# Kernel optimization log

Measured on AMD Instinct MI355X. Metric: run time of the kernel, lower is better.

## Reference

```python
import jax, jax.numpy as jnp
import numpy as np

B, S, DIN, DIM, H = 2, 2304, 1024, 1024, 16
HEAD_DIM = DIM // H            # 64
ROT_DIM = HEAD_DIM             # partial_rotary_factor = 1
BASE = 10000.0
EPS = 1e-6


def setup_inputs() -> dict:
    key = jax.random.key(0)
    ks = jax.random.split(key, 6)
    return {
        "input": jax.random.normal(ks[0], (B, S, DIN), dtype=jnp.float32),
        "qkv_w": jax.random.normal(ks[1], (3 * DIM, DIN), dtype=jnp.float32) * 0.02,
        "qkv_b": jnp.zeros((3 * DIM,), dtype=jnp.float32),
        "q_scale": jnp.ones((DIM,), dtype=jnp.float32),
        "k_scale": jnp.ones((DIM,), dtype=jnp.float32),
        "proj_w": jax.random.normal(ks[2], (DIN, DIM), dtype=jnp.float32) * 0.02,
        "proj_b": jnp.zeros((DIN,), dtype=jnp.float32),
        "height": 48,
        "width": 48,
    }


def _rms_norm(x, scale):
    # RMSNorm over the full inner dim (QKNorm), learned scale
    var = jnp.mean(x * x, axis=-1, keepdims=True)
    return x * jax.lax.rsqrt(var + EPS) * scale


def _rope_1d(x, pos):
    # x: (b, n, h, d_ax), pos: (n,) float; rotate_half-style RoPE
    d = x.shape[-1]
    inv_freq = 1.0 / (BASE ** (jnp.arange(0, d, 2, dtype=jnp.float32) / d))  # (d/2,)
    ang = pos[:, None] * inv_freq                                            # (n, d/2)
    cos = jnp.concatenate([jnp.cos(ang), jnp.cos(ang)], axis=-1)[None, :, None, :]
    sin = jnp.concatenate([jnp.sin(ang), jnp.sin(ang)], axis=-1)[None, :, None, :]
    x1, x2 = jnp.split(x, 2, axis=-1)
    rot = jnp.concatenate([-x2, x1], axis=-1)
    return x * cos + rot * sin


def _rope_2d(x, height, width):
    # axial 2D RoPE: first half of rotary dims keyed by row, second half by col
    n = height * width
    idx = jnp.arange(n, dtype=jnp.float32)
    rows = jnp.floor(idx / width)
    cols = jnp.mod(idx, width)
    half = ROT_DIM // 2
    x_r = _rope_1d(x[..., :half], rows)
    x_c = _rope_1d(x[..., half:ROT_DIM], cols)
    return jnp.concatenate([x_r, x_c, x[..., ROT_DIM:]], axis=-1)


def reference(input, qkv_w, qkv_b, q_scale, k_scale, proj_w, proj_b, height, width):
    b, n, _ = input.shape
    qkv = input @ qkv_w.T + qkv_b                       # (b, n, 3*dim)
    q, k, v = jnp.split(qkv, 3, axis=-1)
    q = _rms_norm(q, q_scale)
    k = _rms_norm(k, k_scale)
    # (b, n, h, d)
    q = q.reshape(b, n, H, HEAD_DIM)
    k = k.reshape(b, n, H, HEAD_DIM)
    v = v.reshape(b, n, H, HEAD_DIM)
    q = _rope_2d(q, height, width)
    k = _rope_2d(k, height, width)
    scale = HEAD_DIM ** (-0.5)
    # (b, h, q, k)
    scores = jnp.einsum("bqhd,bkhd->bhqk", q, k) * scale
    attn = jax.nn.softmax(scores, axis=-1)
    out = jnp.einsum("bhqk,bkhd->bqhd", attn, v)        # (b, n, h, d)
    out = out.reshape(b, n, DIM)
    return out @ proj_w.T + proj_b
```

## Files before the change

kernel.cpp:

```cpp
#include <hip/hip_runtime.h>
#include <math.h>

#define BB   2
#define SS   2304
#define DINC 1024
#define DIMC 1024
#define HH   16
#define HD   64

typedef _Float16 half_t;
typedef __attribute__((ext_vector_type(4))) _Float16 half4;
typedef __attribute__((ext_vector_type(8))) _Float16 half8;
typedef __attribute__((ext_vector_type(4))) float    f32x4;

#define LOG2E 1.44269504088896340736f
#define EXP2(x) __builtin_amdgcn_exp2f(x)

#define GLOAD_LDS16(gp, lp)                                                     \
    __builtin_amdgcn_global_load_lds(                                           \
        (const __attribute__((address_space(1))) void*)(gp),                    \
        (__attribute__((address_space(3))) void*)(lp), 16, 0, 0)

template<int RB>
__device__ __forceinline__
void conv_body(const float* __restrict__ src, half_t* __restrict__ dst,
               int K, int mb, int kb, int t)
{
    constexpr int NG = RB * 32 / 1024;
    const float* sp0 = src + (size_t)mb * RB * K + kb * 32;
    half_t*      dp0 = dst + ((size_t)mb * (K >> 5) + kb) * (RB * 32);
    #pragma unroll
    for (int g = 0; g < NG; ++g) {
        const int e  = g * 1024 + t * 4;
        const int mm = e >> 5, kk = e & 31;
        float4 v = *(const float4*)(sp0 + (size_t)mm * K + kk);
        dp0[e + 0] = (half_t)v.x; dp0[e + 1] = (half_t)v.y;
        dp0[e + 2] = (half_t)v.z; dp0[e + 3] = (half_t)v.w;
    }
}

__global__ __launch_bounds__(256)
void convert_all_f16(const float* __restrict__ input, const float* __restrict__ qkv_w,
                     const float* __restrict__ proj_w, half_t* __restrict__ Ah,
                     half_t* __restrict__ Bh1, half_t* __restrict__ Bh2)
{
    const int bx = blockIdx.x;
    const int kb = blockIdx.y;
    const int t  = threadIdx.x;
    if (bx < 24)      conv_body<192>(input, Ah,  DINC, bx,      kb, t);
    else if (bx < 56) conv_body<96>(qkv_w, Bh1, DINC, bx - 24, kb, t);
    else              conv_body<64>(proj_w, Bh2, DIMC, bx - 56, kb, t);
}

__global__ __launch_bounds__(256, 3)
void gemm_mfma192(const half_t* __restrict__ Ah, const half_t* __restrict__ Bh,
                  const float* __restrict__ bias, half_t* __restrict__ Cout)
{
    const int t    = threadIdx.x;
    const int w    = t >> 6;
    const int lane = t & 63;
    const int l15  = lane & 15, quad = lane >> 4;
    const int wr   = w >> 1;
    const int wc   = w & 1;
    const int mb   = blockIdx.y;
    const int nb   = blockIdx.x;

    __shared__ __align__(16) half_t As[2][6144];
    __shared__ __align__(16) half_t Bs[2][3072];

    f32x4 acc[6][3];
    #pragma unroll
    for (int mt = 0; mt < 6; ++mt)
        #pragma unroll
        for (int nt = 0; nt < 3; ++nt) acc[mt][nt] = (f32x4){0.f, 0.f, 0.f, 0.f};

    const half_t* atile = Ah + (size_t)mb * 32 * 6144;
    const half_t* btile = Bh + (size_t)nb * 32 * 3072;

    for (int kb = 0; kb < 32; kb += 2) {
        #pragma unroll
        for (int u = 0; u < 2; ++u) {
            const half_t* at = atile + (size_t)(kb + u) * 6144;
            const half_t* bt = btile + (size_t)(kb + u) * 3072;
            for (int ch = w; ch < 18; ch += 4) {
                if (ch < 12) GLOAD_LDS16(at + ch * 512 + lane * 8, &As[u][ch * 512]);
                else         GLOAD_LDS16(bt + (ch - 12) * 512 + lane * 8,
                                         &Bs[u][(ch - 12) * 512]);
            }
        }
        __syncthreads();

        #pragma unroll
        for (int u = 0; u < 2; ++u) {
            half8 af[6], bf[3];
            #pragma unroll
            for (int mt = 0; mt < 6; ++mt)
                af[mt] = *(const half8*)(&As[u][(wr * 96 + mt * 16 + l15) * 32 + quad * 8]);
            #pragma unroll
            for (int nt = 0; nt < 3; ++nt)
                bf[nt] = *(const half8*)(&Bs[u][(wc * 48 + nt * 16 + l15) * 32 + quad * 8]);
            #pragma unroll
            for (int mt = 0; mt < 6; ++mt)
                #pragma unroll
                for (int nt = 0; nt < 3; ++nt)
                    acc[mt][nt] = __builtin_amdgcn_mfma_f32_16x16x32_f16(
                        af[mt], bf[nt], acc[mt][nt], 0, 0, 0);
        }
        __syncthreads();
    }

    const int bm = mb * 192, bn = nb * 96;
    #pragma unroll
    for (int nt = 0; nt < 3; ++nt) {
        const int n  = bn + wc * 48 + nt * 16 + l15;
        const float bv = bias[n];
        #pragma unroll
        for (int mt = 0; mt < 6; ++mt) {
            const int m0 = bm + wr * 96 + mt * 16 + quad * 4;
            #pragma unroll
            for (int rg = 0; rg < 4; ++rg)
                Cout[(size_t)(m0 + rg) * 3072 + n] = (half_t)(acc[mt][nt][rg] + bv);
        }
    }
}

template<int BN, bool OUT_HALF>
__global__ __launch_bounds__(256)
void gemm_mfma(const half_t* __restrict__ Ah, const half_t* __restrict__ Bh,
               const float* __restrict__ bias, void* __restrict__ Cout,
               int M, int N, int K)
{
    constexpr int MT = (BN == 128) ? 4 : 2;
    constexpr int NT = 4;
    const int KB = K >> 5;
    __shared__ half_t As[8192];
    __shared__ half_t Bs[2 * BN * 32];

    const int t    = threadIdx.x;
    const int w    = t >> 6;
    const int lane = t & 63;
    const int l15  = lane & 15, quad = lane >> 4;
    const int wr   = (BN == 128) ? (w >> 1) : w;
    const int wc   = (BN == 128) ? (w & 1) : 0;
    const int mb   = blockIdx.y, nb = blockIdx.x;

    f32x4 acc[MT][NT];
    #pragma unroll
    for (int mt = 0; mt < MT; ++mt)
        #pragma unroll
        for (int nt = 0; nt < NT; ++nt) acc[mt][nt] = (f32x4){0.f, 0.f, 0.f, 0.f};

    const half_t* atile = Ah + (size_t)mb * KB * 4096;
    const half_t* btile = Bh + (size_t)nb * KB * (BN * 32);

    for (int kb = 0; kb < KB; kb += 2) {
        #pragma unroll
        for (int u = 0; u < 2; ++u) {
            const half_t* at = atile + (size_t)(kb + u) * 4096;
            const half_t* bt = btile + (size_t)(kb + u) * (BN * 32);
            #pragma unroll
            for (int v = 0; v < 2; ++v) {
                const int ch = w * 2 + v;
                GLOAD_LDS16(at + ch * 512 + lane * 8, As + u * 4096 + ch * 512);
            }
            GLOAD_LDS16(bt + w * 512 + lane * 8, Bs + u * (BN * 32) + w * 512);
        }
        __syncthreads();

        #pragma unroll
        for (int u = 0; u < 2; ++u) {
            half8 af[MT], bf[NT];
            #pragma unroll
            for (int mt = 0; mt < MT; ++mt)
                af[mt] = *(const half8*)(As + u * 4096
                                         + (wr * (MT * 16) + mt * 16 + l15) * 32 + quad * 8);
            #pragma unroll
            for (int nt = 0; nt < NT; ++nt)
                bf[nt] = *(const half8*)(Bs + u * (BN * 32)
                                         + (wc * 64 + nt * 16 + l15) * 32 + quad * 8);
            #pragma unroll
            for (int mt = 0; mt < MT; ++mt)
                #pragma unroll
                for (int nt = 0; nt < NT; ++nt)
                    acc[mt][nt] = __builtin_amdgcn_mfma_f32_16x16x32_f16(
                        af[mt], bf[nt], acc[mt][nt], 0, 0, 0);
        }
        __syncthreads();
    }

    const int bm = mb * 128, bn = nb * BN;
    #pragma unroll
    for (int nt = 0; nt < NT; ++nt) {
        const int n  = bn + wc * 64 + nt * 16 + l15;
        const float bv = bias[n];
        #pragma unroll
        for (int mt = 0; mt < MT; ++mt) {
            const int m0 = bm + wr * (MT * 16) + mt * 16 + quad * 4;
            #pragma unroll
            for (int rg = 0; rg < 4; ++rg) {
                const float v = acc[mt][nt][rg] + bv;
                if (OUT_HALF) ((half_t*)Cout)[(size_t)(m0 + rg) * N + n] = (half_t)v;
                else          ((float*) Cout)[(size_t)(m0 + rg) * N + n] = v;
            }
        }
    }
}

__global__ __launch_bounds__(256)
void normrope_v8(half_t* __restrict__ qkvh, const float* __restrict__ q_scale,
                 const float* __restrict__ k_scale, const int* __restrict__ wptr,
                 half_t* __restrict__ Kf, half_t* __restrict__ Vf)
{
    const int token = blockIdx.x;
    const int s     = token % SS;
    const int b     = token / SS;
    const int w     = *wptr;
    const int t     = threadIdx.x;
    const float rowp = (float)(s / w);
    const float colp = (float)(s % w);

    half_t* base = qkvh + (size_t)token * 3072;

    const int c    = s >> 5;
    const int slot = s & 31;
    const int ktile = (slot >> 2) & 1;
    const int krow  = ((slot >> 3) << 2) + (slot & 3);

    {
        half4 v4 = *(const half4*)(base + 2048 + 4 * t);
        const int dabs0 = 4 * t;
        const int h  = dabs0 >> 6;
        const int sl3 = slot >> 3, sl7 = slot & 7;
        half_t* vdst = Vf + ((size_t)(b * HH + h) * 72 + c) * 2048;
        #pragma unroll
        for (int ii = 0; ii < 4; ++ii) {
            const int d = (dabs0 + ii) & 63;
            vdst[(d >> 4) * 512 + (sl3 * 16 + (d & 15)) * 8 + sl7] = v4[ii];
        }
    }

    __shared__ float buf[DIMC];
    __shared__ float red[4];
    __shared__ __align__(16) half_t obuf[DIMC];

    #pragma unroll
    for (int sel = 0; sel < 2; ++sel) {
        half_t* row = base + sel * DIMC;
        const float* scp = sel ? k_scale : q_scale;

        half4 xh = *(const half4*)(row + 4 * t);
        float x0 = (float)xh[0], x1 = (float)xh[1], x2 = (float)xh[2], x3 = (float)xh[3];
        float ss = x0 * x0 + x1 * x1 + x2 * x2 + x3 * x3;
        #pragma unroll
        for (int o = 32; o >= 1; o >>= 1) ss += __shfl_xor(ss, o);
        if ((t & 63) == 0) red[t >> 6] = ss;
        __syncthreads();

        const float rinv = rsqrtf((red[0] + red[1] + red[2] + red[3]) * (1.0f / DIMC) + 1e-6f);
        float4 g = *(const float4*)(scp + 4 * t);
        buf[4 * t + 0] = x0 * rinv * g.x;
        buf[4 * t + 1] = x1 * rinv * g.y;
        buf[4 * t + 2] = x2 * rinv * g.z;
        buf[4 * t + 3] = x3 * rinv * g.w;
        __syncthreads();

        const float qsc = sel ? 1.0f : (0.125f * LOG2E);

        #pragma unroll
        for (int pp = 0; pp < 2; ++pp) {
            const int p = t + pp * 256;
            const int h = p >> 5;
            const int r = p & 31;
            const int j = r & 15;
            const float pos = (r < 16) ? rowp : colp;
            const int d1 = (r < 16) ? j : (32 + j);
            const int d2 = d1 + 16;
            const float freq = exp2f((float)j * -0.83048202372f);
            const float ang  = pos * freq;
            float sn, cs;
            __sincosf(ang, &sn, &cs);
            const float a1 = buf[h * HD + d1], a2 = buf[h * HD + d2];
            obuf[h * HD + d1] = (half_t)((a1 * cs - a2 * sn) * qsc);
            obuf[h * HD + d2] = (half_t)((a2 * cs + a1 * sn) * qsc);
        }
        __syncthreads();

        if (t < 128) {
            if (sel == 0) {
                *(half8*)(row + t * 8) = *(const half8*)(obuf + t * 8);
            } else {
                const int h = t >> 3, grp = t & 7;
                half_t* kdst = Kf + ((size_t)(b * HH + h) * 72 + c) * 2048;
                const int off = (((ktile << 1) + (grp >> 2)) << 9)
                              + ((((grp & 3) << 4) + krow) << 3);
                *(half8*)(kdst + off) = *(const half8*)(obuf + h * HD + grp * 8);
            }
        }
        __syncthreads();
    }
}

__global__ __launch_bounds__(256, 3)
void flash_attn_mfma17(const half_t* __restrict__ qkvh, const half_t* __restrict__ Kf,
                       const half_t* __restrict__ Vf, half_t* __restrict__ attn_h)
{
    const int flat = blockIdx.x;
    const int xcd  = flat & 7;
    const int idx  = flat >> 3;
    const int bh   = xcd * 4 + idx / 24;
    const int qtb  = idx % 24;
    const int b    = bh >> 4, h = bh & 15;
    const int t    = threadIdx.x;
    const int w    = t >> 6;
    const int qh   = w >> 1;
    const int jt   = w & 1;
    const int lane = t & 63;
    const int l15  = lane & 15, quad = lane >> 4;

    const size_t tb = (size_t)b * SS;
    const int q0 = qtb * 96;

    __shared__ float mlb[4][48];
    __shared__ float Ob[2][64][49];

    half8 qf[3][2];
    #pragma unroll
    for (int qt = 0; qt < 3; ++qt)
        #pragma unroll
        for (int dg = 0; dg < 2; ++dg)
            qf[qt][dg] = *(const half8*)(qkvh + (tb + q0 + qh * 48 + qt * 16 + l15) * 3072
                                          + h * HD + dg * 32 + quad * 8);

    const half8 onesA = (l15 == 0)
        ? (half8){(half_t)1, (half_t)1, (half_t)1, (half_t)1,
                  (half_t)1, (half_t)1, (half_t)1, (half_t)1}
        : (half8){(half_t)0, (half_t)0, (half_t)0, (half_t)0,
                  (half_t)0, (half_t)0, (half_t)0, (half_t)0};

    f32x4 acc[4][3];
    f32x4 acc5[3];
    #pragma unroll
    for (int qt = 0; qt < 3; ++qt) {
        acc5[qt] = (f32x4){0.f, 0.f, 0.f, 0.f};
        #pragma unroll
        for (int dt = 0; dt < 4; ++dt) acc[dt][qt] = (f32x4){0.f, 0.f, 0.f, 0.f};
    }

    const half_t* kpl = Kf + (size_t)bh * 147456 + jt * 2048 + lane * 8;
    const half_t* vpl = Vf + (size_t)bh * 147456 + jt * 2048 + lane * 8;

    half8 k00 = *(const half8*)(kpl);
    half8 k01 = *(const half8*)(kpl + 512);
    half8 k10 = *(const half8*)(kpl + 1024);
    half8 k11 = *(const half8*)(kpl + 1536);
    half8 v0  = *(const half8*)(vpl);
    half8 v1  = *(const half8*)(vpl + 512);
    half8 v2  = *(const half8*)(vpl + 1024);
    half8 v3  = *(const half8*)(vpl + 1536);

    const f32x4 initC = (f32x4){-4.f, -4.f, -4.f, -4.f};

    for (int p = 0; p < 36; ++p) {
        f32x4 scA[3], scB[3];
        __builtin_amdgcn_s_setprio(1);
        #pragma unroll
        for (int qt = 0; qt < 3; ++qt) {
            scA[qt] = initC;
            scA[qt] = __builtin_amdgcn_mfma_f32_16x16x32_f16(k00, qf[qt][0], scA[qt], 0, 0, 0);
            scA[qt] = __builtin_amdgcn_mfma_f32_16x16x32_f16(k01, qf[qt][1], scA[qt], 0, 0, 0);
            scB[qt] = initC;
            scB[qt] = __builtin_amdgcn_mfma_f32_16x16x32_f16(k10, qf[qt][0], scB[qt], 0, 0, 0);
            scB[qt] = __builtin_amdgcn_mfma_f32_16x16x32_f16(k11, qf[qt][1], scB[qt], 0, 0, 0);
        }
        __builtin_amdgcn_s_setprio(0);

        if (p + 1 < 36) {
            const half_t* kN = kpl + (size_t)(p + 1) * 4096;
            k00 = *(const half8*)(kN);
            k01 = *(const half8*)(kN + 512);
            k10 = *(const half8*)(kN + 1024);
            k11 = *(const half8*)(kN + 1536);
        }

        half8 pf[3];
        #pragma unroll
        for (int qt = 0; qt < 3; ++qt) {
            const float a0 = EXP2(scA[qt][0]);
            const float a1 = EXP2(scA[qt][1]);
            const float a2 = EXP2(scA[qt][2]);
            const float a3 = EXP2(scA[qt][3]);
            const float b0 = EXP2(scB[qt][0]);
            const float b1 = EXP2(scB[qt][1]);
            const float b2 = EXP2(scB[qt][2]);
            const float b3 = EXP2(scB[qt][3]);
            pf[qt] = (half8){(half_t)a0, (half_t)a1, (half_t)a2, (half_t)a3,
                             (half_t)b0, (half_t)b1, (half_t)b2, (half_t)b3};
        }

        __builtin_amdgcn_s_setprio(1);
        #pragma unroll
        for (int dt = 0; dt < 4; ++dt) {
            const half8 vf = (dt == 0) ? v0 : (dt == 1) ? v1 : (dt == 2) ? v2 : v3;
            #pragma unroll
            for (int qt = 0; qt < 3; ++qt)
                acc[dt][qt] = __builtin_amdgcn_mfma_f32_16x16x32_f16(
                    vf, pf[qt], acc[dt][qt], 0, 0, 0);
        }
        #pragma unroll
        for (int qt = 0; qt < 3; ++qt)
            acc5[qt] = __builtin_amdgcn_mfma_f32_16x16x32_f16(
                onesA, pf[qt], acc5[qt], 0, 0, 0);
        __builtin_amdgcn_s_setprio(0);

        if (p + 1 < 36) {
            const half_t* vN = vpl + (size_t)(p + 1) * 4096;
            v0 = *(const half8*)(vN);
            v1 = *(const half8*)(vN + 512);
            v2 = *(const half8*)(vN + 1024);
            v3 = *(const half8*)(vN + 1536);
        }
    }

    #pragma unroll
    for (int qt = 0; qt < 3; ++qt)
        if (quad == 0) mlb[w][qt * 16 + l15] = acc5[qt][0];
    __syncthreads();

    float fac[3];
    #pragma unroll
    for (int qt = 0; qt < 3; ++qt) {
        const int q = qt * 16 + l15;
        fac[qt] = 1.0f / (mlb[qh * 2 + 0][q] + mlb[qh * 2 + 1][q]);
    }

    #pragma unroll
    for (int ph = 0; ph < 2; ++ph) {
        if (jt == ph) {
            #pragma unroll
            for (int dt = 0; dt < 4; ++dt)
                #pragma unroll
                for (int qt = 0; qt < 3; ++qt)
                    #pragma unroll
                    for (int rg = 0; rg < 4; ++rg) {
                        const int d = dt * 16 + quad * 4 + rg;
                        const int q = qt * 16 + l15;
                        const float v = acc[dt][qt][rg] * fac[qt];
                        if (ph == 0) Ob[qh][d][q] = v;
                        else         Ob[qh][d][q] += v;
                    }
        }
        __syncthreads();
    }

    #pragma unroll
    for (int g2 = 0; g2 < 3; ++g2) {
        const int q  = g2 * 32 + (t >> 3);
        const int ds = (t & 7) * 8;
        const int qh2 = (q >= 48) ? 1 : 0;
        const int qq  = q - 48 * qh2;
        const size_t mrow = tb + q0 + q;
        const int mb2 = (int)(mrow >> 7);
        const int mm  = (int)(mrow & 127);
        const int kb2 = (h * HD + ds) >> 5;
        const int kk  = ds & 31;
        half8 o;
        #pragma unroll
        for (int ii = 0; ii < 8; ++ii) o[ii] = (half_t)Ob[qh2][ds + ii][qq];
        *(half8*)(attn_h + ((size_t)mb2 * 32 + kb2) * 4096 + mm * 32 + kk) = o;
    }
}

extern "C" void kernel_launch(void* const* d_in, const int* in_sizes, int n_in,
                              void* d_out, int out_size, void* d_ws, size_t ws_size,
                              hipStream_t stream)
{
    const float* input   = (const float*)d_in[0];
    const float* qkv_w   = (const float*)d_in[1];
    const float* qkv_b   = (const float*)d_in[2];
    const float* q_scale = (const float*)d_in[3];
    const float* k_scale = (const float*)d_in[4];
    const float* proj_w  = (const float*)d_in[5];
    const float* proj_b  = (const float*)d_in[6];
    const int*   width   = (const int*)d_in[8];
    float* out = (float*)d_out;

    half_t* qkvh   = (half_t*)d_ws;
    half_t* attn_h = qkvh   + (size_t)4608 * 3072;
    half_t* Vf     = attn_h + (size_t)4608 * 1024;
    half_t* Ah     = Vf     + (size_t)32 * 72 * 2048;
    half_t* Bh1    = Ah     + (size_t)4608 * 1024;
    half_t* Bh2    = Bh1    + (size_t)3072 * 1024;
    half_t* Kf     = Ah;

    const int M = BB * SS;

    convert_all_f16<<<dim3(72, 32), 256, 0, stream>>>(input, qkv_w, proj_w,
                                                      Ah, Bh1, Bh2);

    gemm_mfma192<<<dim3(3 * DIMC / 96, M / 192), 256, 0, stream>>>(
        Ah, Bh1, qkv_b, qkvh);

    normrope_v8<<<M, 256, 0, stream>>>(qkvh, q_scale, k_scale, width, Kf, Vf);

    flash_attn_mfma17<<<dim3(768), 256, 0, stream>>>(qkvh, Kf, Vf, attn_h);

    gemm_mfma<64, false><<<dim3(DINC / 64, M / 128), 256, 0, stream>>>(
        attn_h, Bh2, proj_b, out, M, DINC, DIMC);
}
```

Before: 228.9 us.

## Double-buffer QKV GEMM k-loop and stage epilogue through LDS

The 192x96-tile QKV GEMM now prefetches the next k-slab into the alternate LDS buffer while computing on the current one, so each step needs one barrier instead of two per pair of steps. The epilogue writes bias-added fp16 results into shared memory first and then stores them to global memory as coalesced 16-byte vectors, replacing scattered 2-byte stores. The LDS footprint stays the same because one flat buffer is reused for the A/B tiles and the output staging. The risk is that a barrier every k-step can cost more than the old pairwise loop.

```diff
diff --git a/kernel.cpp b/kernel.cpp
--- a/kernel.cpp
+++ b/kernel.cpp
@@ -65,8 +65,7 @@
     const int mb   = blockIdx.y;
     const int nb   = blockIdx.x;
 
-    __shared__ __align__(16) half_t As[2][6144];
-    __shared__ __align__(16) half_t Bs[2][3072];
+    __shared__ __align__(16) half_t smem[18432];
 
     f32x4 acc[6][3];
     #pragma unroll
@@ -77,50 +76,68 @@
     const half_t* atile = Ah + (size_t)mb * 32 * 6144;
     const half_t* btile = Bh + (size_t)nb * 32 * 3072;
 
-    for (int kb = 0; kb < 32; kb += 2) {
-        #pragma unroll
-        for (int u = 0; u < 2; ++u) {
-            const half_t* at = atile + (size_t)(kb + u) * 6144;
-            const half_t* bt = btile + (size_t)(kb + u) * 3072;
-            for (int ch = w; ch < 18; ch += 4) {
-                if (ch < 12) GLOAD_LDS16(at + ch * 512 + lane * 8, &As[u][ch * 512]);
-                else         GLOAD_LDS16(bt + (ch - 12) * 512 + lane * 8,
-                                         &Bs[u][(ch - 12) * 512]);
-            }
-        }
-        __syncthreads();
-
-        #pragma unroll
-        for (int u = 0; u < 2; ++u) {
-            half8 af[6], bf[3];
-            #pragma unroll
-            for (int mt = 0; mt < 6; ++mt)
-                af[mt] = *(const half8*)(&As[u][(wr * 96 + mt * 16 + l15) * 32 + quad * 8]);
+    #define STAGE192(s, bsel)                                                   \
+    {                                                                           \
+        const half_t* at = atile + (size_t)(s) * 6144;                          \
+        const half_t* bt = btile + (size_t)(s) * 3072;                          \
+        half_t* dstA = smem + (bsel) * 9216;                                    \
+        half_t* dstB = dstA + 6144;                                             \
+        for (int ch = w; ch < 18; ch += 4) {                                    \
+            if (ch < 12) GLOAD_LDS16(at + ch * 512 + lane * 8, dstA + ch * 512);\
+            else         GLOAD_LDS16(bt + (ch - 12) * 512 + lane * 8,           \
+                                     dstB + (ch - 12) * 512);                   \
+        }                                                                       \
+    }
+
+    STAGE192(0, 0);
+    __syncthreads();
+
+    for (int s = 0; s < 32; ++s) {
+        const int b = s & 1;
+        if (s + 1 < 32) STAGE192(s + 1, b ^ 1);
+
+        const half_t* Au = smem + b * 9216;
+        const half_t* Bu = Au + 6144;
+        half8 af[6], bf[3];
+        #pragma unroll
+        for (int mt = 0; mt < 6; ++mt)
+            af[mt] = *(const half8*)(Au + (wr * 96 + mt * 16 + l15) * 32 + quad * 8);
+        #pragma unroll
+        for (int nt = 0; nt < 3; ++nt)
+            bf[nt] = *(const half8*)(Bu + (wc * 48 + nt * 16 + l15) * 32 + quad * 8);
+        #pragma unroll
+        for (int mt = 0; mt < 6; ++mt)
             #pragma unroll
             for (int nt = 0; nt < 3; ++nt)
-                bf[nt] = *(const half8*)(&Bs[u][(wc * 48 + nt * 16 + l15) * 32 + quad * 8]);
-            #pragma unroll
-            for (int mt = 0; mt < 6; ++mt)
-                #pragma unroll
-                for (int nt = 0; nt < 3; ++nt)
-                    acc[mt][nt] = __builtin_amdgcn_mfma_f32_16x16x32_f16(
-                        af[mt], bf[nt], acc[mt][nt], 0, 0, 0);
-        }
-        __syncthreads();
-    }
+                acc[mt][nt] = __builtin_amdgcn_mfma_f32_16x16x32_f16(
+                    af[mt], bf[nt], acc[mt][nt], 0, 0, 0);
+
+        __syncthreads();
+    }
+    #undef STAGE192
 
     const int bm = mb * 192, bn = nb * 96;
     #pragma unroll
     for (int nt = 0; nt < 3; ++nt) {
-        const int n  = bn + wc * 48 + nt * 16 + l15;
-        const float bv = bias[n];
+        const int lc = wc * 48 + nt * 16 + l15;
+        const float bv = bias[bn + lc];
         #pragma unroll
         for (int mt = 0; mt < 6; ++mt) {
-            const int m0 = bm + wr * 96 + mt * 16 + quad * 4;
+            const int lr0 = wr * 96 + mt * 16 + quad * 4;
             #pragma unroll
             for (int rg = 0; rg < 4; ++rg)
-                Cout[(size_t)(m0 + rg) * 3072 + n] = (half_t)(acc[mt][nt][rg] + bv);
-        }
+                smem[(lr0 + rg) * 96 + lc] = (half_t)(acc[mt][nt][rg] + bv);
+        }
+    }
+    __syncthreads();
+
+    #pragma unroll
+    for (int i = 0; i < 9; ++i) {
+        const int g   = t + 256 * i;
+        const int lr  = g / 12;
+        const int lc8 = (g % 12) * 8;
+        *(half8*)(Cout + (size_t)(bm + lr) * 3072 + bn + lc8)
+            = *(const half8*)(smem + lr * 96 + lc8);
     }
 }
 
```

Measured after the change: 224.8 us. Within noise of the previous version (-1.8%).
